# Kernel tuning notes

Measured on AMD Instinct MI355X. Metric: run time of the kernel, lower is better.

The kernel has to match this reference:

```python
import jax, jax.numpy as jnp
import numpy as np
import math

NUM_HEADS = 16


def setup_inputs() -> dict:
    key = jax.random.key(0)
    ks = jax.random.split(key, 7)
    B, S, D = 2, 2048, 1024
    scale = 1.0 / math.sqrt(D)
    return {
        "query": jax.random.normal(ks[0], (B, S, D), jnp.float32),
        "key": jax.random.normal(ks[1], (B, S, D), jnp.float32),
        "value": jax.random.normal(ks[2], (B, S, D), jnp.float32),
        "Wq": jax.random.normal(ks[3], (D, D), jnp.float32) * scale,
        "Wk": jax.random.normal(ks[4], (D, D), jnp.float32) * scale,
        "Wv": jax.random.normal(ks[5], (D, D), jnp.float32) * scale,
        "Wo": jax.random.normal(ks[6], (D, D), jnp.float32) * scale,
    }


def reference(query, key, value, Wq, Wk, Wv, Wo):
    B, Sq, D = query.shape
    Sk = key.shape[1]
    H = NUM_HEADS
    dk = D // H
    # torch Linear (no bias): y = x @ W.T
    q = (query @ Wq.T).reshape(B, Sq, H, dk).transpose(0, 2, 1, 3)  # [B,H,Sq,dk]
    k = (key @ Wk.T).reshape(B, Sk, H, dk).transpose(0, 2, 1, 3)
    v = (value @ Wv.T).reshape(B, Sk, H, dk).transpose(0, 2, 1, 3)
    scores = jnp.einsum("bhqd,bhkd->bhqk", q, k) / jnp.sqrt(jnp.float32(dk))
    causal = jnp.tril(jnp.ones((Sq, Sk), dtype=bool))  # mask_future=True
    scores = jnp.where(causal[None, None], scores, jnp.float32(-1e9))
    p = jax.nn.softmax(scores, axis=-1)
    x = jnp.einsum("bhqk,bhkd->bhqd", p, v)  # [B,H,Sq,dk]
    x = x.transpose(0, 2, 1, 3).reshape(B, Sq, D)
    return x @ Wo.T
```

## Files before the change

### kernel.cpp

```cpp
#include <hip/hip_runtime.h>
#include <hip/hip_bf16.h>
#include <stdint.h>

#define D_MODEL 1024
#define NHEADS  16
#define DK      64
#define SEQ     2048
#define BATCH   2

typedef __bf16 bf16x8 __attribute__((ext_vector_type(8)));
typedef __bf16 bf16x4 __attribute__((ext_vector_type(4)));
typedef float  f32x4  __attribute__((ext_vector_type(4)));

__device__ __forceinline__ void async_copy16(const void* g, void* l) {
  __builtin_amdgcn_global_load_lds(
      (__attribute__((address_space(1))) void*)g,
      (__attribute__((address_space(3))) void*)l, 16, 0, 0);
}

__global__ void cast_all(const float* __restrict__ q, const float* __restrict__ k,
                         const float* __restrict__ v, const float* __restrict__ wq,
                         const float* __restrict__ wk, const float* __restrict__ wv,
                         const float* __restrict__ wo,
                         __bf16* __restrict__ oq, __bf16* __restrict__ ok,
                         __bf16* __restrict__ ov, __bf16* __restrict__ owq,
                         __bf16* __restrict__ owk, __bf16* __restrict__ owv,
                         __bf16* __restrict__ owo) {
  constexpr unsigned Q4 = (unsigned)(BATCH * SEQ * D_MODEL) / 4;
  constexpr unsigned W4 = (unsigned)(D_MODEL * D_MODEL) / 4;
  unsigned i = blockIdx.x * 256u + threadIdx.x;
  const float* in; __bf16* out; unsigned off;
  if (i < 3 * Q4) {
    unsigned z = i >> 20; off = i & (Q4 - 1);
    in  = z == 0 ? q : z == 1 ? k : v;
    out = z == 0 ? oq : z == 1 ? ok : ov;
  } else {
    unsigned j = i - 3 * Q4;
    unsigned z = j >> 18; off = j & (W4 - 1);
    in  = z == 0 ? wq : z == 1 ? wk : z == 2 ? wv : wo;
    out = z == 0 ? owq : z == 1 ? owk : z == 2 ? owv : owo;
  }
  float4 val = *(const float4*)(in + (size_t)off * 4);
  bf16x4 o;
  o.x = (__bf16)val.x; o.y = (__bf16)val.y; o.z = (__bf16)val.z; o.w = (__bf16)val.w;
  *(bf16x4*)(out + (size_t)off * 4) = o;
}

__global__ __launch_bounds__(256, 3)
void gemm_proj(const __bf16* __restrict__ A0, const __bf16* __restrict__ A1, const __bf16* __restrict__ A2,
               const __bf16* __restrict__ B0, const __bf16* __restrict__ B1, const __bf16* __restrict__ B2,
               __bf16* __restrict__ Qp, __bf16* __restrict__ Kp, __bf16* __restrict__ Vt) {
  constexpr int K = D_MODEL, N = D_MODEL;
  const int zi = blockIdx.z;
  const __bf16* A; const __bf16* Bm;
  if (zi == 0)      { A = A0; Bm = B0; }
  else if (zi == 1) { A = A1; Bm = B1; }
  else              { A = A2; Bm = B2; }

  __shared__ __bf16 Ash[128 * 32];
  __shared__ __bf16 Bsh[128 * 32];
  __shared__ __align__(16) __bf16 Tr[128 * 136];

  const int tid  = threadIdx.x;
  const int lane = tid & 63;
  const int w    = tid >> 6;
  const int quad = lane >> 4;
  const int l16  = lane & 15;
  const int wr   = w >> 1, wc = w & 1;
  const size_t m0 = (size_t)blockIdx.x * 128;
  const size_t n0 = (size_t)blockIdx.y * 128;

  f32x4 acc[4][4] = {};

  for (int k0 = 0; k0 < K; k0 += 32) {
#pragma unroll
    for (int it = 0; it < 2; ++it) {
      int slot = tid + it * 256;
      async_copy16(A + (m0 + (slot >> 2)) * K + k0 + (slot & 3) * 8, &Ash[slot * 8]);
    }
#pragma unroll
    for (int it = 0; it < 2; ++it) {
      int slot = tid + it * 256;
      async_copy16(Bm + (n0 + (slot >> 2)) * K + k0 + (slot & 3) * 8, &Bsh[slot * 8]);
    }
    __syncthreads();
    bf16x8 af[4], bfr[4];
#pragma unroll
    for (int i = 0; i < 4; ++i)
      af[i] = *(const bf16x8*)&Ash[(wr * 64 + i * 16 + l16) * 32 + quad * 8];
#pragma unroll
    for (int j = 0; j < 4; ++j)
      bfr[j] = *(const bf16x8*)&Bsh[(wc * 64 + j * 16 + l16) * 32 + quad * 8];
#pragma unroll
    for (int i = 0; i < 4; ++i)
#pragma unroll
      for (int j = 0; j < 4; ++j)
        acc[i][j] = __builtin_amdgcn_mfma_f32_16x16x32_bf16(af[i], bfr[j], acc[i][j], 0, 0, 0);
    __syncthreads();
  }

  if (zi != 2) {
    __bf16* C = (zi == 0) ? Qp : Kp;
#pragma unroll
    for (int i = 0; i < 4; ++i)
#pragma unroll
      for (int j = 0; j < 4; ++j)
#pragma unroll
        for (int r = 0; r < 4; ++r) {
          size_t row = m0 + wr * 64 + i * 16 + quad * 4 + r;
          size_t col = n0 + wc * 64 + j * 16 + l16;
          C[row * N + col] = (__bf16)acc[i][j][r];
        }
  } else {
#pragma unroll
    for (int i = 0; i < 4; ++i)
#pragma unroll
      for (int j = 0; j < 4; ++j)
#pragma unroll
        for (int r = 0; r < 4; ++r)
          Tr[(wc * 64 + j * 16 + l16) * 136 + (wr * 64 + i * 16 + quad * 4 + r)] =
              (__bf16)acc[i][j][r];
    __syncthreads();
    const int b_  = (int)(m0 >> 11);
    const int sl0 = (int)(m0 & 2047);
#pragma unroll
    for (int it = 0; it < 8; ++it) {
      int slot = tid + it * 256;
      int d = slot >> 4, sc = slot & 15;
      *(int4*)&Vt[((size_t)(b_ * D_MODEL) + n0 + d) * SEQ + sl0 + sc * 8] =
          *(const int4*)&Tr[d * 136 + sc * 8];
    }
  }
}

__global__ __launch_bounds__(256, 2)
void gemm_out(const __bf16* __restrict__ A, const __bf16* __restrict__ Bm,
              float* __restrict__ C) {
  constexpr int BM = 64, BN = 128, K = D_MODEL, N = D_MODEL;
  __shared__ __bf16 Ash[BM * 32];
  __shared__ __bf16 Bsh[BN * 32];

  const int tid  = threadIdx.x;
  const int lane = tid & 63;
  const int w    = tid >> 6;
  const int quad = lane >> 4;
  const int l16  = lane & 15;
  const int wr   = w >> 1, wc = w & 1;
  const size_t m0 = (size_t)blockIdx.x * BM;
  const size_t n0 = (size_t)blockIdx.y * BN;

  f32x4 acc[2][4] = {};

  for (int k0 = 0; k0 < K; k0 += 32) {
    {
      int slot = tid;
      async_copy16(A + (m0 + (slot >> 2)) * K + k0 + (slot & 3) * 8, &Ash[slot * 8]);
    }
#pragma unroll
    for (int it = 0; it < 2; ++it) {
      int slot = tid + it * 256;
      async_copy16(Bm + (n0 + (slot >> 2)) * K + k0 + (slot & 3) * 8, &Bsh[slot * 8]);
    }
    __syncthreads();
    bf16x8 af[2], bfr[4];
#pragma unroll
    for (int i = 0; i < 2; ++i)
      af[i] = *(const bf16x8*)&Ash[(wr * 32 + i * 16 + l16) * 32 + quad * 8];
#pragma unroll
    for (int j = 0; j < 4; ++j)
      bfr[j] = *(const bf16x8*)&Bsh[(wc * 64 + j * 16 + l16) * 32 + quad * 8];
#pragma unroll
    for (int i = 0; i < 2; ++i)
#pragma unroll
      for (int j = 0; j < 4; ++j)
        acc[i][j] = __builtin_amdgcn_mfma_f32_16x16x32_bf16(af[i], bfr[j], acc[i][j], 0, 0, 0);
    __syncthreads();
  }

#pragma unroll
  for (int i = 0; i < 2; ++i)
#pragma unroll
    for (int j = 0; j < 4; ++j)
#pragma unroll
      for (int r = 0; r < 4; ++r) {
        size_t row = m0 + wr * 32 + i * 16 + quad * 4 + r;
        size_t col = n0 + wc * 64 + j * 16 + l16;
        C[row * N + col] = acc[i][j][r];
      }
}

#define PS_W 40

__global__ __launch_bounds__(256, 3)
void attn_kernel(const __bf16* __restrict__ Qp, const __bf16* __restrict__ Kp,
                 const __bf16* __restrict__ Vt, __bf16* __restrict__ Xo) {
  __shared__ __bf16 Kb[2 * 2 * 64 * 32];
  __shared__ __bf16 Vb[2 * 2 * 64 * 32];
  __shared__ __bf16 Ps[4 * 32 * PS_W];
  __shared__ float  Xch[2 * 16 * 66];
  __shared__ float  Lsum[2 * 32];

  const int tid  = threadIdx.x;
  const int lane = tid & 63;
  const int w    = tid >> 6;
  const int qh   = w >> 1, kh = w & 1;
  const int quad = lane >> 4;
  const int l16  = lane & 15;
  const int bh   = blockIdx.x;
  const int qt   = 31 - blockIdx.y;
  const int b    = bh >> 4, h = bh & 15;
  const int q0   = qt * 64;
  const size_t baseRow = (size_t)b * SEQ;
  const int colBase = h * DK;

  const int srow = w * 16 + (lane >> 2);
  const int sk   = (lane & 3) * 8;
  const int skz  = (((lane & 3) ^ ((lane >> 3) & 3)) * 8);
  const int swz  = (l16 >> 1) & 3;

  const float c1 = 0.18033688011f;
  const float c2 = -23.083120654f;

  bf16x8 aq[2][2];
  {
    const __bf16* qrow = Qp + (baseRow + q0 + qh * 32 + l16) * D_MODEL + colBase;
#pragma unroll
    for (int mt = 0; mt < 2; ++mt)
#pragma unroll
      for (int kd = 0; kd < 2; ++kd)
        aq[mt][kd] = *(const bf16x8*)(qrow + (size_t)mt * 16 * D_MODEL + kd * 32 + quad * 8);
  }

  f32x4 oacc[2][4] = {};
  float plsum[2][4] = {};

  {
    const __bf16* kbase = Kp + (baseRow + srow) * D_MODEL + colBase + skz;
    async_copy16(kbase,      &Kb[0 * 2048 + srow * 32 + sk]);
    async_copy16(kbase + 32, &Kb[1 * 2048 + srow * 32 + sk]);
    const __bf16* vbase = Vt + ((size_t)b * D_MODEL + colBase + srow) * SEQ + skz;
    async_copy16(vbase,      &Vb[0 * 2048 + srow * 32 + sk]);
    async_copy16(vbase + 32, &Vb[1 * 2048 + srow * 32 + sk]);
  }

  for (int j = 0; j <= qt; ++j) {
    const int bf = j & 1;
    __syncthreads();

    if (j < qt) {
      const int nb = bf ^ 1;
      const __bf16* kbase = Kp + (baseRow + (size_t)(j + 1) * 64 + srow) * D_MODEL + colBase + skz;
      async_copy16(kbase,      &Kb[(nb * 2 + 0) * 2048 + srow * 32 + sk]);
      async_copy16(kbase + 32, &Kb[(nb * 2 + 1) * 2048 + srow * 32 + sk]);
      const __bf16* vbase = Vt + ((size_t)b * D_MODEL + colBase + srow) * SEQ + (size_t)(j + 1) * 64 + skz;
      async_copy16(vbase,      &Vb[(nb * 2 + 0) * 2048 + srow * 32 + sk]);
      async_copy16(vbase + 32, &Vb[(nb * 2 + 1) * 2048 + srow * 32 + sk]);
    }

    f32x4 sacc[2][2] = {};
    __builtin_amdgcn_s_setprio(1);
#pragma unroll
    for (int kd = 0; kd < 2; ++kd) {
      bf16x8 bk0 = *(const bf16x8*)&Kb[(bf * 2 + kd) * 2048 + (kh * 32 + l16) * 32 + (quad ^ swz) * 8];
      bf16x8 bk1 = *(const bf16x8*)&Kb[(bf * 2 + kd) * 2048 + (kh * 32 + 16 + l16) * 32 + (quad ^ swz) * 8];
      sacc[0][0] = __builtin_amdgcn_mfma_f32_16x16x32_bf16(aq[0][kd], bk0, sacc[0][0], 0, 0, 0);
      sacc[0][1] = __builtin_amdgcn_mfma_f32_16x16x32_bf16(aq[0][kd], bk1, sacc[0][1], 0, 0, 0);
      sacc[1][0] = __builtin_amdgcn_mfma_f32_16x16x32_bf16(aq[1][kd], bk0, sacc[1][0], 0, 0, 0);
      sacc[1][1] = __builtin_amdgcn_mfma_f32_16x16x32_bf16(aq[1][kd], bk1, sacc[1][1], 0, 0, 0);
    }
    __builtin_amdgcn_s_setprio(0);

    const bool diag = (j == qt);
#pragma unroll
    for (int mt = 0; mt < 2; ++mt)
#pragma unroll
      for (int nt2 = 0; nt2 < 2; ++nt2)
#pragma unroll
        for (int r = 0; r < 4; ++r) {
          float arg = fmaf(sacc[mt][nt2][r], c1, c2);
          if (diag) {
            int rowg = q0 + qh * 32 + mt * 16 + quad * 4 + r;
            int colg = j * 64 + kh * 32 + nt2 * 16 + l16;
            if (colg > rowg) arg = -1e30f;
          }
          float p = __builtin_amdgcn_exp2f(arg);
          plsum[mt][r] += p;
          Ps[(w * 32 + mt * 16 + quad * 4 + r) * PS_W + nt2 * 16 + l16] = (__bf16)p;
        }

    bf16x8 bv[4];
    __builtin_amdgcn_s_setprio(1);
#pragma unroll
    for (int nt = 0; nt < 4; ++nt)
      bv[nt] = *(const bf16x8*)&Vb[(bf * 2 + kh) * 2048 + (nt * 16 + l16) * 32 + (quad ^ swz) * 8];
#pragma unroll
    for (int mt = 0; mt < 2; ++mt) {
      bf16x8 ap = *(const bf16x8*)&Ps[(w * 32 + mt * 16 + l16) * PS_W + quad * 8];
#pragma unroll
      for (int nt = 0; nt < 4; ++nt)
        oacc[mt][nt] = __builtin_amdgcn_mfma_f32_16x16x32_bf16(ap, bv[nt], oacc[mt][nt], 0, 0, 0);
    }
    __builtin_amdgcn_s_setprio(0);
  }

  float lred[2][4];
#pragma unroll
  for (int mt = 0; mt < 2; ++mt)
#pragma unroll
    for (int r = 0; r < 4; ++r) {
      float l = plsum[mt][r];
      for (int off = 1; off < 16; off <<= 1) l += __shfl_xor(l, off, 64);
      lred[mt][r] = l;
    }

#pragma unroll
  for (int mt = 0; mt < 2; ++mt) {
    __syncthreads();
    if (kh == 1) {
#pragma unroll
      for (int nt = 0; nt < 4; ++nt)
#pragma unroll
        for (int r = 0; r < 4; ++r)
          Xch[(qh * 16 + quad * 4 + r) * 66 + nt * 16 + l16] = oacc[mt][nt][r];
#pragma unroll
      for (int r = 0; r < 4; ++r)
        Lsum[qh * 32 + mt * 16 + quad * 4 + r] = lred[mt][r];
    }
    __syncthreads();
    if (kh == 0) {
#pragma unroll
      for (int r = 0; r < 4; ++r) {
        float lt  = lred[mt][r] + Lsum[qh * 32 + mt * 16 + quad * 4 + r];
        float inv = 1.0f / lt;
        size_t row = baseRow + q0 + qh * 32 + mt * 16 + quad * 4 + r;
#pragma unroll
        for (int nt = 0; nt < 4; ++nt) {
          float o = oacc[mt][nt][r] + Xch[(qh * 16 + quad * 4 + r) * 66 + nt * 16 + l16];
          Xo[row * D_MODEL + colBase + nt * 16 + l16] = (__bf16)(o * inv);
        }
      }
    }
  }
}

extern "C" void kernel_launch(void* const* d_in, const int* in_sizes, int n_in,
                              void* d_out, int out_size, void* d_ws, size_t ws_size,
                              hipStream_t stream) {
  const float* q  = (const float*)d_in[0];
  const float* k  = (const float*)d_in[1];
  const float* v  = (const float*)d_in[2];
  const float* wq = (const float*)d_in[3];
  const float* wk = (const float*)d_in[4];
  const float* wv = (const float*)d_in[5];
  const float* wo = (const float*)d_in[6];
  float* out = (float*)d_out;

  const size_t MD = (size_t)BATCH * SEQ * D_MODEL;
  const size_t WD = (size_t)D_MODEL * D_MODEL;
  __bf16* ws  = (__bf16*)d_ws;
  __bf16* Qp  = ws;
  __bf16* Kp  = Qp + MD;
  __bf16* Vt  = Kp + MD;
  __bf16* Xa  = Vt + MD;
  __bf16* qbf = Xa + MD;
  __bf16* kbf = qbf + MD;
  __bf16* vbf = kbf + MD;
  __bf16* wqb = vbf + MD;
  __bf16* wkb = wqb + WD;
  __bf16* wvb = wkb + WD;
  __bf16* wob = wvb + WD;

  cast_all<<<16384, 256, 0, stream>>>(q, k, v, wq, wk, wv, wo,
                                      qbf, kbf, vbf, wqb, wkb, wvb, wob);

  gemm_proj<<<dim3(32, 8, 3), 256, 0, stream>>>(
      qbf, kbf, vbf, wqb, wkb, wvb, Qp, Kp, Vt);

  attn_kernel<<<dim3(BATCH * NHEADS, 32), 256, 0, stream>>>(Qp, Kp, Vt, Xa);

  gemm_out<<<dim3(64, 8), 256, 0, stream>>>(Xa, wob, out);
}
```

Baseline: 201.0 us.

## Double GEMM K-tile to 64 with XOR-swizzled LDS layout and aliased transpose buffer

Measured after the change: 193.1 us. -3.9%, faster.

```diff
diff --git a/kernel.cpp b/kernel.cpp
--- a/kernel.cpp
+++ b/kernel.cpp
@@ -57,9 +57,10 @@
   else if (zi == 1) { A = A1; Bm = B1; }
   else              { A = A2; Bm = B2; }
 
-  __shared__ __bf16 Ash[128 * 32];
-  __shared__ __bf16 Bsh[128 * 32];
-  __shared__ __align__(16) __bf16 Tr[128 * 136];
+  __shared__ __align__(16) char smem[34816];
+  __bf16* Ash = (__bf16*)smem;
+  __bf16* Bsh = (__bf16*)(smem + 16384);
+  __bf16* Tr  = (__bf16*)smem;
 
   const int tid  = threadIdx.x;
   const int lane = tid & 63;
@@ -72,30 +73,39 @@
 
   f32x4 acc[4][4] = {};
 
-  for (int k0 = 0; k0 < K; k0 += 32) {
-#pragma unroll
-    for (int it = 0; it < 2; ++it) {
+  for (int k0 = 0; k0 < K; k0 += 64) {
+#pragma unroll
+    for (int it = 0; it < 4; ++it) {
       int slot = tid + it * 256;
-      async_copy16(A + (m0 + (slot >> 2)) * K + k0 + (slot & 3) * 8, &Ash[slot * 8]);
-    }
-#pragma unroll
-    for (int it = 0; it < 2; ++it) {
+      int row = slot >> 3, ch = slot & 7;
+      async_copy16(A + (m0 + row) * K + k0 + ((ch ^ (row & 7)) * 8), &Ash[slot * 8]);
+    }
+#pragma unroll
+    for (int it = 0; it < 4; ++it) {
       int slot = tid + it * 256;
-      async_copy16(Bm + (n0 + (slot >> 2)) * K + k0 + (slot & 3) * 8, &Bsh[slot * 8]);
-    }
-    __syncthreads();
-    bf16x8 af[4], bfr[4];
-#pragma unroll
-    for (int i = 0; i < 4; ++i)
-      af[i] = *(const bf16x8*)&Ash[(wr * 64 + i * 16 + l16) * 32 + quad * 8];
-#pragma unroll
-    for (int j = 0; j < 4; ++j)
-      bfr[j] = *(const bf16x8*)&Bsh[(wc * 64 + j * 16 + l16) * 32 + quad * 8];
-#pragma unroll
-    for (int i = 0; i < 4; ++i)
-#pragma unroll
-      for (int j = 0; j < 4; ++j)
-        acc[i][j] = __builtin_amdgcn_mfma_f32_16x16x32_bf16(af[i], bfr[j], acc[i][j], 0, 0, 0);
+      int row = slot >> 3, ch = slot & 7;
+      async_copy16(Bm + (n0 + row) * K + k0 + ((ch ^ (row & 7)) * 8), &Bsh[slot * 8]);
+    }
+    __syncthreads();
+#pragma unroll
+    for (int kk = 0; kk < 2; ++kk) {
+      bf16x8 af[4], bfr[4];
+#pragma unroll
+      for (int i = 0; i < 4; ++i) {
+        int row = wr * 64 + i * 16 + l16;
+        af[i] = *(const bf16x8*)&Ash[row * 64 + (((kk * 4 + quad) ^ (row & 7)) * 8)];
+      }
+#pragma unroll
+      for (int j = 0; j < 4; ++j) {
+        int row = wc * 64 + j * 16 + l16;
+        bfr[j] = *(const bf16x8*)&Bsh[row * 64 + (((kk * 4 + quad) ^ (row & 7)) * 8)];
+      }
+#pragma unroll
+      for (int i = 0; i < 4; ++i)
+#pragma unroll
+        for (int j = 0; j < 4; ++j)
+          acc[i][j] = __builtin_amdgcn_mfma_f32_16x16x32_bf16(af[i], bfr[j], acc[i][j], 0, 0, 0);
+    }
     __syncthreads();
   }
 
@@ -137,8 +147,8 @@
 void gemm_out(const __bf16* __restrict__ A, const __bf16* __restrict__ Bm,
               float* __restrict__ C) {
   constexpr int BM = 64, BN = 128, K = D_MODEL, N = D_MODEL;
-  __shared__ __bf16 Ash[BM * 32];
-  __shared__ __bf16 Bsh[BN * 32];
+  __shared__ __bf16 Ash[BM * 64];
+  __shared__ __bf16 Bsh[BN * 64];
 
   const int tid  = threadIdx.x;
   const int lane = tid & 63;
@@ -151,29 +161,39 @@
 
   f32x4 acc[2][4] = {};
 
-  for (int k0 = 0; k0 < K; k0 += 32) {
-    {
-      int slot = tid;
-      async_copy16(A + (m0 + (slot >> 2)) * K + k0 + (slot & 3) * 8, &Ash[slot * 8]);
-    }
+  for (int k0 = 0; k0 < K; k0 += 64) {
 #pragma unroll
     for (int it = 0; it < 2; ++it) {
       int slot = tid + it * 256;
-      async_copy16(Bm + (n0 + (slot >> 2)) * K + k0 + (slot & 3) * 8, &Bsh[slot * 8]);
-    }
-    __syncthreads();
-    bf16x8 af[2], bfr[4];
-#pragma unroll
-    for (int i = 0; i < 2; ++i)
-      af[i] = *(const bf16x8*)&Ash[(wr * 32 + i * 16 + l16) * 32 + quad * 8];
-#pragma unroll
-    for (int j = 0; j < 4; ++j)
-      bfr[j] = *(const bf16x8*)&Bsh[(wc * 64 + j * 16 + l16) * 32 + quad * 8];
-#pragma unroll
-    for (int i = 0; i < 2; ++i)
-#pragma unroll
-      for (int j = 0; j < 4; ++j)
-        acc[i][j] = __builtin_amdgcn_mfma_f32_16x16x32_bf16(af[i], bfr[j], acc[i][j], 0, 0, 0);
+      int row = slot >> 3, ch = slot & 7;
+      async_copy16(A + (m0 + row) * K + k0 + ((ch ^ (row & 7)) * 8), &Ash[slot * 8]);
+    }
+#pragma unroll
+    for (int it = 0; it < 4; ++it) {
+      int slot = tid + it * 256;
+      int row = slot >> 3, ch = slot & 7;
+      async_copy16(Bm + (n0 + row) * K + k0 + ((ch ^ (row & 7)) * 8), &Bsh[slot * 8]);
+    }
+    __syncthreads();
+#pragma unroll
+    for (int kk = 0; kk < 2; ++kk) {
+      bf16x8 af[2], bfr[4];
+#pragma unroll
+      for (int i = 0; i < 2; ++i) {
+        int row = wr * 32 + i * 16 + l16;
+        af[i] = *(const bf16x8*)&Ash[row * 64 + (((kk * 4 + quad) ^ (row & 7)) * 8)];
+      }
+#pragma unroll
+      for (int j = 0; j < 4; ++j) {
+        int row = wc * 64 + j * 16 + l16;
+        bfr[j] = *(const bf16x8*)&Bsh[row * 64 + (((kk * 4 + quad) ^ (row & 7)) * 8)];
+      }
+#pragma unroll
+      for (int i = 0; i < 2; ++i)
+#pragma unroll
+        for (int j = 0; j < 4; ++j)
+          acc[i][j] = __builtin_amdgcn_mfma_f32_16x16x32_bf16(af[i], bfr[j], acc[i][j], 0, 0, 0);
+    }
     __syncthreads();
   }
 
```
